# Performance work log

Measured on AMD Instinct MI355X. Metric: run time of the kernel, lower is better.

The kernel has to match this reference:

```python
import jax, jax.numpy as jnp
import numpy as np

HIDDEN = 4096
N_HEADS = 32
HEAD_DIM = HIDDEN // N_HEADS  # 128
ROPE_BASE = 10000.0


def _rotate_half(x):
    h = x.shape[-1] // 2
    return jnp.concatenate((-x[..., h:], x[..., :h]), axis=-1)


def _rope_sin_cos(position_ids):
    # position_ids: [B, S] int -> sin, cos: [B, 1, S, head_dim]
    inv_freq = 1.0 / (ROPE_BASE ** (jnp.arange(0, HEAD_DIM, 2, dtype=jnp.float32) / HEAD_DIM))
    freqs = position_ids.astype(jnp.float32)[..., None] * inv_freq  # [B,S,hd/2]
    emb = jnp.concatenate((freqs, freqs), axis=-1)  # [B,S,hd]
    return jnp.sin(emb)[:, None, :, :], jnp.cos(emb)[:, None, :, :]


def setup_inputs() -> dict:
    key = jax.random.key(0)
    k1, k2, k3 = jax.random.split(key, 3)
    B, S = 2, 2048
    hidden_states = jax.random.normal(k1, (B, S, HIDDEN), dtype=jnp.float32)
    w_qkv = jax.random.normal(k2, (HIDDEN, 3 * HIDDEN), dtype=jnp.float32) * 0.02
    wo = jax.random.normal(k3, (HIDDEN, HIDDEN), dtype=jnp.float32) * 0.02
    position_ids = jnp.broadcast_to(jnp.arange(S, dtype=jnp.int32)[None, :], (B, S))
    return {"hidden_states": hidden_states, "w_qkv": w_qkv, "wo": wo,
            "position_ids": position_ids}


def reference(hidden_states, w_qkv, wo, position_ids):
    B, S, H = hidden_states.shape
    qkv = hidden_states @ w_qkv  # [B,S,3H]
    q, k, v = jnp.split(qkv, 3, axis=-1)
    # [B,S,nH,hd] -> [B,nH,S,hd]
    q = q.reshape(B, S, N_HEADS, HEAD_DIM).transpose(0, 2, 1, 3)
    k = k.reshape(B, S, N_HEADS, HEAD_DIM).transpose(0, 2, 1, 3)
    v = v.reshape(B, S, N_HEADS, HEAD_DIM).transpose(0, 2, 1, 3)
    sin, cos = _rope_sin_cos(position_ids)  # [B,1,S,hd]
    q = q * cos + _rotate_half(q) * sin
    k = k * cos + _rotate_half(k) * sin
    scale = 1.0 / np.sqrt(HEAD_DIM)
    scores = jnp.einsum('bhqd,bhkd->bhqk', q, k) * scale
    causal = jnp.tril(jnp.ones((S, S), dtype=bool))
    scores = jnp.where(causal[None, None, :, :], scores, jnp.finfo(scores.dtype).min)
    attn = jax.nn.softmax(scores, axis=-1)
    out = jnp.einsum('bhqk,bhkd->bhqd', attn, v)  # [B,nH,S,hd]
    out = out.transpose(0, 2, 1, 3).reshape(B, S, H)
    return out @ wo
```

## Files before the change

### kernel.cpp

```cpp
#include <hip/hip_runtime.h>

typedef unsigned int u32;
typedef unsigned short u16;
typedef short short8 __attribute__((ext_vector_type(8)));
typedef float f32x4 __attribute__((ext_vector_type(4)));
typedef unsigned short us4 __attribute__((ext_vector_type(4)));

#define S_LEN 2048
#define BATCH 2
#define HID 4096
#define NH 32
#define HD 128
#define TRIH 12288

#define GCAST(p) ((const __attribute__((address_space(1))) u32*)(p))
#define LCAST(p) ((__attribute__((address_space(3))) u32*)(p))

static __device__ __forceinline__ u16 f2bf(float f) {
  union { float f; u32 u; } x; x.f = f;
  u32 u = x.u;
  u32 r = u + 0x7FFFu + ((u >> 16) & 1u);
  return (u16)(r >> 16);
}
static __device__ __forceinline__ float bf2f(u16 h) {
  union { u32 u; float f; } x; x.u = ((u32)h) << 16;
  return x.f;
}

__global__ __launch_bounds__(256) void cvt_f32_bf16(const float* __restrict__ in,
                                                    u16* __restrict__ out, int n4) {
  int i = blockIdx.x * 256 + threadIdx.x;
  if (i >= n4) return;
  float4 v = ((const float4*)in)[i];
  us4 o;
  o.x = f2bf(v.x); o.y = f2bf(v.y); o.z = f2bf(v.z); o.w = f2bf(v.w);
  ((us4*)out)[i] = o;
}

__global__ __launch_bounds__(256) void tr_cvt(const float* __restrict__ in,
                                              u16* __restrict__ out, int R, int C) {
  __shared__ float tile[32][33];
  int c0 = blockIdx.x * 32, r0 = blockIdx.y * 32;
  int tx = threadIdx.x, ty = threadIdx.y;
  for (int i = ty; i < 32; i += 8)
    tile[i][tx] = in[(size_t)(r0 + i) * C + c0 + tx];
  __syncthreads();
  for (int i = ty; i < 32; i += 8)
    out[(size_t)(c0 + i) * R + r0 + tx] = f2bf(tile[tx][i]);
}


template<int MQ, int NQ>
static __device__ __forceinline__ void mfma_quad(f32x4 (&acc)[8][4], short8 (&af)[4][2],
                                                 short8 (&bfr)[4][2]) {
#pragma unroll
  for (int ml = 0; ml < 4; ++ml)
#pragma unroll
    for (int nl = 0; nl < 2; ++nl) {
      acc[MQ*4+ml][NQ*2+nl] = __builtin_amdgcn_mfma_f32_16x16x32_bf16(
          af[ml][0], bfr[NQ*2+nl][0], acc[MQ*4+ml][NQ*2+nl], 0, 0, 0);
      acc[MQ*4+ml][NQ*2+nl] = __builtin_amdgcn_mfma_f32_16x16x32_bf16(
          af[ml][1], bfr[NQ*2+nl][1], acc[MQ*4+ml][NQ*2+nl], 0, 0, 0);
    }
}

template<int MQ>
static __device__ __forceinline__ void read_a(short8 (&af)[4][2], const u16* abase, int lane) {
#pragma unroll
  for (int ml = 0; ml < 4; ++ml) {
    int r = MQ*64 + ml*16 + (lane & 15);
#pragma unroll
    for (int kh = 0; kh < 2; ++kh) {
      int j = kh*4 + (lane >> 4);
      af[ml][kh] = *(const short8*)(abase + r*64 + ((j ^ (r & 7)) << 3));
    }
  }
}
template<int NQ>
static __device__ __forceinline__ void read_b(short8 (&bfr)[4][2], const u16* bbase,
                                              int rbase, int lane) {
#pragma unroll
  for (int nl = 0; nl < 2; ++nl) {
    int r = rbase + (NQ*2+nl)*16 + (lane & 15);
#pragma unroll
    for (int kh = 0; kh < 2; ++kh) {
      int j = kh*4 + (lane >> 4);
      bfr[NQ*2+nl][kh] = *(const short8*)(bbase + r*64 + ((j ^ (r & 7)) << 3));
    }
  }
}

#define BAR_MFMA(MQX, NQX) \
  __builtin_amdgcn_s_barrier(); \
  asm volatile("s_waitcnt lgkmcnt(0)" ::: "memory"); \
  __builtin_amdgcn_sched_barrier(0); \
  __builtin_amdgcn_s_setprio(1); \
  mfma_quad<MQX, NQX>(acc, af, bfr); \
  __builtin_amdgcn_s_setprio(0); \
  __builtin_amdgcn_s_barrier();

#define SEAM(N) \
  asm volatile("s_waitcnt vmcnt(" #N ")" ::: "memory"); \
  __builtin_amdgcn_s_barrier(); \
  __builtin_amdgcn_sched_barrier(0);

template<int OUTF32>
__global__ __launch_bounds__(512, 1) void gemm256(const u16* __restrict__ A,
                                                  const u16* __restrict__ Bt,
                                                  void* __restrict__ Cout,
                                                  int M, int N, int K, int nbx) {
  __shared__ __attribute__((aligned(16))) u16 lds[65536];
  const int tid = threadIdx.x, wave = tid >> 6, lane = tid & 63;
  const int wr = wave >> 2, wc = wave & 3;
  const int nwg = gridDim.x, wg = blockIdx.x, cpx = nwg >> 3;
  const int swz = (wg & 7) * cpx + (wg >> 3);
  const size_t tileM = (size_t)(swz / nbx) * 256;
  const size_t tileN = (size_t)(swz % nbx) * 256;
  const int nIter = K >> 7;

  const int r_ = tid >> 3;
  const int gc_ = (tid & 7) ^ (r_ & 7);

  const u16* Ag = A + tileM * K;
  const u16* Bg = Bt + tileN * K;

  f32x4 acc[8][4] = {};
  short8 af[4][2], bfr[4][2];

  auto stageA = [&](int kt, int buf, int half) {
    const u16* g0 = Ag + (size_t)(half*128 + r_) * K + kt*64 + (gc_ << 3);
    u16* l = lds + buf*16384 + half*8192 + wave*512;
    __builtin_amdgcn_global_load_lds(GCAST(g0), LCAST(l), 16, 0, 0);
    __builtin_amdgcn_global_load_lds(GCAST(g0 + (size_t)64*K), LCAST(l + 4096), 16, 0, 0);
  };
  auto stageB = [&](int kt, int buf, int half) {
    const u16* g0 = Bg + (size_t)(half*128 + r_) * K + kt*64 + (gc_ << 3);
    u16* l = lds + 32768 + buf*16384 + half*8192 + wave*512;
    __builtin_amdgcn_global_load_lds(GCAST(g0), LCAST(l), 16, 0, 0);
    __builtin_amdgcn_global_load_lds(GCAST(g0 + (size_t)64*K), LCAST(l + 4096), 16, 0, 0);
  };

  const u16* a0 = lds + wr*8192;
  const u16* a1 = lds + 16384 + wr*8192;
  const u16* b0 = lds + 32768 + (wc >> 1)*8192;
  const u16* b1 = lds + 32768 + 16384 + (wc >> 1)*8192;
  const int brb = (wc & 1) * 64;

  stageA(0, 0, 0); stageA(0, 0, 1);
  stageB(0, 0, 0); stageB(0, 0, 1);
  stageB(1, 1, 0); stageB(1, 1, 1);

  for (int i = 0; i < nIter; ++i) {
    const int t1 = 2*i + 1, t2 = 2*i + 2, t3 = 2*i + 3;
    const bool more = (i + 1 < nIter);
    SEAM(4)
    read_a<0>(af, a0, lane);
    read_b<0>(bfr, b0, brb, lane);
    stageA(t1, 1, 0);
    asm volatile("s_waitcnt lgkmcnt(8)" ::: "memory");
    BAR_MFMA(0, 0)
    read_b<1>(bfr, b0, brb, lane);
    stageA(t1, 1, 1);
    BAR_MFMA(0, 1)
    read_a<1>(af, a0, lane);
    if (more) stageB(t2, 0, 0);
    BAR_MFMA(1, 0)
    if (more) stageB(t2, 0, 1);
    BAR_MFMA(1, 1)
    if (more) { SEAM(4) } else { SEAM(0) }
    read_a<0>(af, a1, lane);
    read_b<0>(bfr, b1, brb, lane);
    if (more) stageA(t2, 0, 0);
    asm volatile("s_waitcnt lgkmcnt(8)" ::: "memory");
    BAR_MFMA(0, 0)
    read_b<1>(bfr, b1, brb, lane);
    if (more) stageA(t2, 0, 1);
    BAR_MFMA(0, 1)
    read_a<1>(af, a1, lane);
    if (more) stageB(t3, 1, 0);
    BAR_MFMA(1, 0)
    if (more) stageB(t3, 1, 1);
    BAR_MFMA(1, 1)
  }

  const int r0o = (lane >> 4) << 2, c0o = lane & 15;
#pragma unroll
  for (int m = 0; m < 8; ++m)
#pragma unroll
    for (int n = 0; n < 4; ++n)
#pragma unroll
      for (int rr = 0; rr < 4; ++rr) {
        size_t grow = tileM + wr*128 + m*16 + r0o + rr;
        size_t gcol = tileN + wc*64 + n*16 + c0o;
        if (OUTF32) ((float*)Cout)[grow * N + gcol] = acc[m][n][rr];
        else        ((u16*)Cout)[grow * N + gcol] = f2bf(acc[m][n][rr]);
      }
}

__global__ __launch_bounds__(256) void rope_kernel(u16* __restrict__ qkv,
                                                   const int* __restrict__ pid) {
  int idx = blockIdx.x * 256 + threadIdx.x;
  int row = idx >> 12;
  int rem = idx & 4095;
  int which = rem >> 11;
  int rem2 = rem & 2047;
  int h = rem2 >> 6;
  int j = rem2 & 63;
  u16* p = qkv + (size_t)row * TRIH + which * HID + h * HD + j;
  float x0 = bf2f(p[0]), x1 = bf2f(p[64]);
  float pos = (float)pid[row];
  float invf = expf(-(float)j * 0.14391156831212787f);
  float th = pos * invf;
  float sn, cs;
  sincosf(th, &sn, &cs);
  p[0]  = f2bf(x0 * cs - x1 * sn);
  p[64] = f2bf(x1 * cs + x0 * sn);
}

__global__ __launch_bounds__(256) void attn_kernel(const u16* __restrict__ qkv,
                                                   u16* __restrict__ O) {
  const int bid = blockIdx.x;
  const int qt = 31 - (bid >> 6);
  const int bh = bid & 63;
  const int b = bh >> 5, h = bh & 31;
  const int tid = threadIdx.x, wave = tid >> 6, lane = tid & 63;
  __shared__ u16 Ks[64 * 128];
  __shared__ u16 VsT[128 * 64];
  __shared__ u16 Ps[4][16 * 64];
  const u16* base = qkv + (size_t)b * S_LEN * TRIH + h * HD;

  const int rbase = (lane >> 4) << 2;
  const int cbase = lane & 15;
  const int q_lo = qt * 64;

  short8 qf[4];
  {
    const u16* qrow = base + (size_t)(q_lo + wave * 16 + cbase) * TRIH;
#pragma unroll
    for (int f = 0; f < 4; ++f)
      qf[f] = *(const short8*)(qrow + ((f * 4 + (lane >> 4)) << 3));
  }

  float mrun[4], lrun[4];
  f32x4 accO[8] = {};
#pragma unroll
  for (int r = 0; r < 4; ++r) { mrun[r] = -1e30f; lrun[r] = 0.f; }

  short8 kreg[4], vreg[4];
#pragma unroll
  for (int it = 0; it < 4; ++it) {
    int c = tid + it * 256;
    int row = c >> 4, ch = c & 15;
    const u16* src = base + (size_t)row * TRIH + (ch << 3);
    kreg[it] = *(const short8*)(src + HID);
    vreg[it] = *(const short8*)(src + 2 * HID);
  }

  for (int t = 0; t <= qt; ++t) {
    __syncthreads();
#pragma unroll
    for (int it = 0; it < 4; ++it) {
      int c = tid + it * 256;
      int row = c >> 4, ch = c & 15;
      *(short8*)(Ks + row * 128 + ((ch ^ (row & 7)) << 3)) = kreg[it];
#pragma unroll
      for (int i = 0; i < 8; ++i) {
        int d = (ch << 3) + i;
        VsT[d * 64 + (((row >> 3) ^ (ch & 7)) << 3) + (row & 7)] = (u16)vreg[it][i];
      }
    }
    __syncthreads();

    if (t < qt) {
      int kv1 = (t + 1) << 6;
#pragma unroll
      for (int it = 0; it < 4; ++it) {
        int c = tid + it * 256;
        int row = c >> 4, ch = c & 15;
        const u16* src = base + (size_t)(kv1 + row) * TRIH + (ch << 3);
        kreg[it] = *(const short8*)(src + HID);
        vreg[it] = *(const short8*)(src + 2 * HID);
      }
    }

    f32x4 s[4] = {};
#pragma unroll
    for (int n = 0; n < 4; ++n) {
      int krow = n * 16 + cbase;
#pragma unroll
      for (int f = 0; f < 4; ++f) {
        int ch = f * 4 + (lane >> 4);
        short8 kf = *(const short8*)(Ks + krow * 128 + ((ch ^ (krow & 7)) << 3));
        s[n] = __builtin_amdgcn_mfma_f32_16x16x32_bf16(qf[f], kf, s[n], 0, 0, 0);
      }
    }
    const float scale = 0.08838834764831845f;
    const int kv0 = t << 6;
    if (t == qt) {
#pragma unroll
      for (int n = 0; n < 4; ++n)
#pragma unroll
        for (int r = 0; r < 4; ++r) {
          int kvcol = kv0 + n * 16 + cbase;
          int qrow = q_lo + wave * 16 + rbase + r;
          s[n][r] = (kvcol <= qrow) ? s[n][r] * scale : -1e30f;
        }
    } else {
#pragma unroll
      for (int n = 0; n < 4; ++n) s[n] *= scale;
    }

    float tmax[4];
#pragma unroll
    for (int r = 0; r < 4; ++r) {
      float tm = fmaxf(fmaxf(s[0][r], s[1][r]), fmaxf(s[2][r], s[3][r]));
      tm = fmaxf(tm, __shfl_xor(tm, 1));
      tm = fmaxf(tm, __shfl_xor(tm, 2));
      tm = fmaxf(tm, __shfl_xor(tm, 4));
      tm = fmaxf(tm, __shfl_xor(tm, 8));
      tmax[r] = tm;
    }
    bool need = false;
#pragma unroll
    for (int r = 0; r < 4; ++r) need |= (tmax[r] > mrun[r] + 8.0f);
    if (__any(need)) {
#pragma unroll
      for (int r = 0; r < 4; ++r) {
        float mnew = fmaxf(mrun[r], tmax[r]);
        float corr = __expf(mrun[r] - mnew);
        float rs = 0.f;
#pragma unroll
        for (int n = 0; n < 4; ++n) { float pv = __expf(s[n][r] - mnew); s[n][r] = pv; rs += pv; }
        rs += __shfl_xor(rs, 1); rs += __shfl_xor(rs, 2);
        rs += __shfl_xor(rs, 4); rs += __shfl_xor(rs, 8);
        lrun[r] = lrun[r] * corr + rs;
        mrun[r] = mnew;
#pragma unroll
        for (int nd = 0; nd < 8; ++nd) accO[nd][r] *= corr;
      }
    } else {
#pragma unroll
      for (int r = 0; r < 4; ++r) {
        float rs = 0.f;
#pragma unroll
        for (int n = 0; n < 4; ++n) { float pv = __expf(s[n][r] - mrun[r]); s[n][r] = pv; rs += pv; }
        rs += __shfl_xor(rs, 1); rs += __shfl_xor(rs, 2);
        rs += __shfl_xor(rs, 4); rs += __shfl_xor(rs, 8);
        lrun[r] += rs;
      }
    }

    u16* Pw = (u16*)Ps[wave];
#pragma unroll
    for (int n = 0; n < 4; ++n)
#pragma unroll
      for (int r = 0; r < 4; ++r) {
        int rl = rbase + r;
        int col = n * 16 + cbase;
        Pw[rl * 64 + (((col >> 3) ^ (rl & 7)) << 3) + (col & 7)] = f2bf(s[n][r]);
      }

    short8 pa[2];
    {
      int prow = lane & 15;
#pragma unroll
      for (int f2 = 0; f2 < 2; ++f2) {
        int ch = f2 * 4 + (lane >> 4);
        pa[f2] = *(const short8*)(Pw + prow * 64 + ((ch ^ (prow & 7)) << 3));
      }
    }
#pragma unroll
    for (int nd = 0; nd < 8; ++nd) {
      int drow = nd * 16 + cbase;
#pragma unroll
      for (int f2 = 0; f2 < 2; ++f2) {
        int ch = f2 * 4 + (lane >> 4);
        short8 vb = *(const short8*)(VsT + drow * 64 + ((ch ^ ((drow >> 3) & 7)) << 3));
        accO[nd] = __builtin_amdgcn_mfma_f32_16x16x32_bf16(pa[f2], vb, accO[nd], 0, 0, 0);
      }
    }
  }

#pragma unroll
  for (int nd = 0; nd < 8; ++nd)
#pragma unroll
    for (int r = 0; r < 4; ++r) {
      int qrow = q_lo + wave * 16 + rbase + r;
      int col = h * HD + nd * 16 + cbase;
      O[(size_t)(b * S_LEN + qrow) * HID + col] = f2bf(accO[nd][r] / lrun[r]);
    }
}

extern "C" void kernel_launch(void* const* d_in, const int* in_sizes, int n_in,
                              void* d_out, int out_size, void* d_ws, size_t ws_size,
                              hipStream_t stream) {
  const float* hidden = (const float*)d_in[0];
  const float* w_qkv  = (const float*)d_in[1];
  const float* wo     = (const float*)d_in[2];
  const int*   pid    = (const int*)d_in[3];

  const size_t MB = 1024ull * 1024ull;
  u16* hb    = (u16*)d_ws;
  u16* wqkvT = (u16*)((char*)d_ws + 32 * MB);
  u16* woT   = (u16*)((char*)d_ws + 128 * MB);
  u16* qkvb  = (u16*)((char*)d_ws + 160 * MB);
  u16* Obuf  = hb;

  cvt_f32_bf16<<<16384, 256, 0, stream>>>(hidden, hb, (BATCH * S_LEN * HID) / 4);
  dim3 tb(32, 8);
  tr_cvt<<<dim3(TRIH / 32, HID / 32), tb, 0, stream>>>(w_qkv, wqkvT, HID, TRIH);
  tr_cvt<<<dim3(HID / 32, HID / 32), tb, 0, stream>>>(wo, woT, HID, HID);

  gemm256<0><<<768, 512, 0, stream>>>(hb, wqkvT, qkvb, BATCH * S_LEN, TRIH, HID, TRIH / 256);

  rope_kernel<<<(BATCH * S_LEN * 2 * NH * 64) / 256, 256, 0, stream>>>(qkvb, pid);

  attn_kernel<<<2048, 256, 0, stream>>>(qkvb, Obuf);

  gemm256<1><<<256, 512, 0, stream>>>(Obuf, woT, d_out, BATCH * S_LEN, HID, HID, HID / 256);
}
```

Measured before the change: 843.7 us.

## Double attention query tile per block and fold GEMM wait into MFMA barrier

The attention kernel now uses 512 threads handling 128 query rows per block, so every K/V tile staged in shared memory is reused by twice as many waves. The grid is halved, and waves in the lower half skip the last KV tile through a per-wave limit. Separately, the GEMM's vmcnt wait and barrier at the loop seam are merged into the final MFMA phase's closing barrier, removing one barrier per half-iteration. The risks are idle waves on the diagonal tile, tighter register budgets under launch_bounds(512,6), and fewer blocks for load balance.

```diff
diff --git a/kernel.cpp b/kernel.cpp
--- a/kernel.cpp
+++ b/kernel.cpp
@@ -99,8 +99,14 @@
   __builtin_amdgcn_s_setprio(0); \
   __builtin_amdgcn_s_barrier();
 
-#define SEAM(N) \
-  asm volatile("s_waitcnt vmcnt(" #N ")" ::: "memory"); \
+#define BAR_MFMA_DRAIN(MQX, NQX, NSTR) \
+  __builtin_amdgcn_s_barrier(); \
+  asm volatile("s_waitcnt lgkmcnt(0)" ::: "memory"); \
+  __builtin_amdgcn_sched_barrier(0); \
+  __builtin_amdgcn_s_setprio(1); \
+  mfma_quad<MQX, NQX>(acc, af, bfr); \
+  __builtin_amdgcn_s_setprio(0); \
+  asm volatile("s_waitcnt vmcnt(" NSTR ")" ::: "memory"); \
   __builtin_amdgcn_s_barrier(); \
   __builtin_amdgcn_sched_barrier(0);
 
@@ -149,11 +155,13 @@
   stageA(0, 0, 0); stageA(0, 0, 1);
   stageB(0, 0, 0); stageB(0, 0, 1);
   stageB(1, 1, 0); stageB(1, 1, 1);
+  asm volatile("s_waitcnt vmcnt(4)" ::: "memory");
+  __builtin_amdgcn_s_barrier();
+  __builtin_amdgcn_sched_barrier(0);
 
   for (int i = 0; i < nIter; ++i) {
     const int t1 = 2*i + 1, t2 = 2*i + 2, t3 = 2*i + 3;
     const bool more = (i + 1 < nIter);
-    SEAM(4)
     read_a<0>(af, a0, lane);
     read_b<0>(bfr, b0, brb, lane);
     stageA(t1, 1, 0);
@@ -165,9 +173,12 @@
     read_a<1>(af, a0, lane);
     if (more) stageB(t2, 0, 0);
     BAR_MFMA(1, 0)
-    if (more) stageB(t2, 0, 1);
-    BAR_MFMA(1, 1)
-    if (more) { SEAM(4) } else { SEAM(0) }
+    if (more) {
+      stageB(t2, 0, 1);
+      BAR_MFMA_DRAIN(1, 1, "4")
+    } else {
+      BAR_MFMA_DRAIN(1, 1, "0")
+    }
     read_a<0>(af, a1, lane);
     read_b<0>(bfr, b1, brb, lane);
     if (more) stageA(t2, 0, 0);
@@ -179,8 +190,12 @@
     read_a<1>(af, a1, lane);
     if (more) stageB(t3, 1, 0);
     BAR_MFMA(1, 0)
-    if (more) stageB(t3, 1, 1);
-    BAR_MFMA(1, 1)
+    if (more) {
+      stageB(t3, 1, 1);
+      BAR_MFMA_DRAIN(1, 1, "4")
+    } else {
+      BAR_MFMA(1, 1)
+    }
   }
 
   const int r0o = (lane >> 4) << 2, c0o = lane & 15;
@@ -217,50 +232,54 @@
   p[64] = f2bf(x1 * cs + x0 * sn);
 }
 
-__global__ __launch_bounds__(256) void attn_kernel(const u16* __restrict__ qkv,
-                                                   u16* __restrict__ O) {
+__global__ __launch_bounds__(512, 6) void attn_kernel(const u16* __restrict__ qkv,
+                                                      u16* __restrict__ O) {
   const int bid = blockIdx.x;
-  const int qt = 31 - (bid >> 6);
+  const int qt = 15 - (bid >> 6);
   const int bh = bid & 63;
   const int b = bh >> 5, h = bh & 31;
   const int tid = threadIdx.x, wave = tid >> 6, lane = tid & 63;
   __shared__ u16 Ks[64 * 128];
   __shared__ u16 VsT[128 * 64];
-  __shared__ u16 Ps[4][16 * 64];
+  __shared__ u16 Ps[8][16 * 64];
   const u16* base = qkv + (size_t)b * S_LEN * TRIH + h * HD;
 
   const int rbase = (lane >> 4) << 2;
   const int cbase = lane & 15;
-  const int q_lo = qt * 64;
+  const int q_lo = qt * 128;
+  const int wrow0 = q_lo + wave * 16;
 
   short8 qf[4];
   {
-    const u16* qrow = base + (size_t)(q_lo + wave * 16 + cbase) * TRIH;
+    const u16* qrow = base + (size_t)(wrow0 + cbase) * TRIH;
 #pragma unroll
     for (int f = 0; f < 4; ++f)
       qf[f] = *(const short8*)(qrow + ((f * 4 + (lane >> 4)) << 3));
   }
 
+  const int tmax_w = 2 * qt + (wave >= 4 ? 1 : 0);
+  const int tmax_b = 2 * qt + 1;
+
   float mrun[4], lrun[4];
   f32x4 accO[8] = {};
 #pragma unroll
   for (int r = 0; r < 4; ++r) { mrun[r] = -1e30f; lrun[r] = 0.f; }
 
-  short8 kreg[4], vreg[4];
-#pragma unroll
-  for (int it = 0; it < 4; ++it) {
-    int c = tid + it * 256;
+  short8 kreg[2], vreg[2];
+#pragma unroll
+  for (int it = 0; it < 2; ++it) {
+    int c = tid + it * 512;
     int row = c >> 4, ch = c & 15;
     const u16* src = base + (size_t)row * TRIH + (ch << 3);
     kreg[it] = *(const short8*)(src + HID);
     vreg[it] = *(const short8*)(src + 2 * HID);
   }
 
-  for (int t = 0; t <= qt; ++t) {
+  for (int t = 0; t <= tmax_b; ++t) {
     __syncthreads();
 #pragma unroll
-    for (int it = 0; it < 4; ++it) {
-      int c = tid + it * 256;
+    for (int it = 0; it < 2; ++it) {
+      int c = tid + it * 512;
       int row = c >> 4, ch = c & 15;
       *(short8*)(Ks + row * 128 + ((ch ^ (row & 7)) << 3)) = kreg[it];
 #pragma unroll
@@ -271,11 +290,11 @@
     }
     __syncthreads();
 
-    if (t < qt) {
+    if (t < tmax_b) {
       int kv1 = (t + 1) << 6;
 #pragma unroll
-      for (int it = 0; it < 4; ++it) {
-        int c = tid + it * 256;
+      for (int it = 0; it < 2; ++it) {
+        int c = tid + it * 512;
         int row = c >> 4, ch = c & 15;
         const u16* src = base + (size_t)(kv1 + row) * TRIH + (ch << 3);
         kreg[it] = *(const short8*)(src + HID);
@@ -283,6 +302,8 @@
       }
     }
 
+    if (t > tmax_w) continue;
+
     f32x4 s[4] = {};
 #pragma unroll
     for (int n = 0; n < 4; ++n) {
@@ -296,13 +317,13 @@
     }
     const float scale = 0.08838834764831845f;
     const int kv0 = t << 6;
-    if (t == qt) {
+    if (t == tmax_w) {
 #pragma unroll
       for (int n = 0; n < 4; ++n)
 #pragma unroll
         for (int r = 0; r < 4; ++r) {
           int kvcol = kv0 + n * 16 + cbase;
-          int qrow = q_lo + wave * 16 + rbase + r;
+          int qrow = wrow0 + rbase + r;
           s[n][r] = (kvcol <= qrow) ? s[n][r] * scale : -1e30f;
         }
     } else {
@@ -385,7 +406,7 @@
   for (int nd = 0; nd < 8; ++nd)
 #pragma unroll
     for (int r = 0; r < 4; ++r) {
-      int qrow = q_lo + wave * 16 + rbase + r;
+      int qrow = wrow0 + rbase + r;
       int col = h * HD + nd * 16 + cbase;
       O[(size_t)(b * S_LEN + qrow) * HID + col] = f2bf(accO[nd][r] / lrun[r]);
     }
@@ -415,7 +436,7 @@
 
   rope_kernel<<<(BATCH * S_LEN * 2 * NH * 64) / 256, 256, 0, stream>>>(qkvb, pid);
 
-  attn_kernel<<<2048, 256, 0, stream>>>(qkvb, Obuf);
+  attn_kernel<<<1024, 512, 0, stream>>>(qkvb, Obuf);
 
   gemm256<1><<<256, 512, 0, stream>>>(Obuf, woT, d_out, BATCH * S_LEN, HID, HID, HID / 256);
 }
```

New measurement: 1.703 ms. 102% more time.
